# Optimization experiments

Measured on AMD Instinct MI355X. Metric: run time of the kernel, lower is better.

Reference implementation:

```python
import jax, jax.numpy as jnp
import numpy as np

C, H, W, D, M = 64, 512, 512, 4, 16


def setup_inputs() -> dict:
    key = jax.random.key(0)
    ks = jax.random.split(key, 9)
    scale = (1.0 / (C * C)) ** 0.5
    return {
        "q": jax.random.normal(ks[0], (1, 1, H, W), jnp.float32),
        "proj_w": jax.random.normal(ks[1], (C, 1, 1, 1), jnp.float32),
        "proj_b": jax.random.normal(ks[2], (C, 1, 1), jnp.float32) * 0.01,
        "spec_wr": jax.random.normal(ks[3], (D, C, C, M, M), jnp.float32) * scale,
        "spec_wi": jax.random.normal(ks[4], (D, C, C, M, M), jnp.float32) * scale,
        "w_w": jax.random.normal(ks[5], (D, C, C, 1, 1), jnp.float32) * (1.0 / C ** 0.5),
        "w_b": jax.random.normal(ks[6], (D, C, 1, 1), jnp.float32) * 0.01,
        "final_w": jax.random.normal(ks[7], (1, C, 1, 1), jnp.float32) * (1.0 / C ** 0.5),
        "final_b": jax.random.normal(ks[8], (1, 1, 1), jnp.float32) * 0.01,
    }


def _spectral(x, wr, wi, m):
    # x: (C,H,W). FFT2 -> contract low modes -> zero-pad -> iFFT2, take real part.
    Cin, Hh, Ww = x.shape
    x_ft = jnp.fft.fft2(x, axes=(-2, -1))  # (C,H,W) complex
    w = (wr + 1j * wi).astype(x_ft.dtype)  # (Cin,Cout,m,m)
    out_sub = jnp.einsum('imn,iomn->omn', x_ft[:, :m, :m], w)
    out_ft = jnp.zeros((wr.shape[1], Hh, Ww), dtype=x_ft.dtype).at[:, :m, :m].set(out_sub)
    return jnp.fft.ifft2(out_ft, axes=(-2, -1)).real


def reference(q, proj_w, proj_b, spec_wr, spec_wi, w_w, w_b, final_w, final_b):
    m = spec_wr.shape[-1]
    depth = spec_wr.shape[0]
    x = q[0].astype(jnp.float32)  # (C_in,H,W) -- batch must be 1
    # 1x1 conv lift
    x = jnp.einsum('oi,ihw->ohw', proj_w[:, :, 0, 0], x) + proj_b
    for d in range(depth):
        x_spec = _spectral(x, spec_wr[d], spec_wi[d], m)
        x_local = jnp.einsum('oi,ihw->ohw', w_w[d, :, :, 0, 0], x) + w_b[d]
        x = jax.nn.gelu(x_spec + x_local)
    x = jnp.einsum('oi,ihw->ohw', final_w[:, :, 0, 0], x) + final_b
    return x[None]  # re-add batch dim
```

## Files before the change

### kernel.cpp

```cpp
#include <hip/hip_runtime.h>
#include <cmath>

#define CC 64
#define HH 512
#define WWID 512
#define HWSZ (HH*WWID)
#define DEPTH 4

typedef __attribute__((ext_vector_type(8))) short short8;
typedef __attribute__((ext_vector_type(4))) float floatx4;

__device__ inline unsigned short f2bf(float f){
  unsigned int u = __float_as_uint(f);
  u += 0x7FFF + ((u >> 16) & 1);
  return (unsigned short)(u >> 16);
}
__device__ inline float bf2f(unsigned short h){
  return __uint_as_float(((unsigned int)h) << 16);
}

__global__ void k_init(const float* __restrict__ ww,
                       float* __restrict__ ctab, float* __restrict__ stab,
                       unsigned short* __restrict__ trigBh, unsigned short* __restrict__ trigBl,
                       unsigned short* __restrict__ trigTh, unsigned short* __restrict__ trigTl,
                       unsigned short* __restrict__ Whi, unsigned short* __restrict__ Wlo,
                       float4* __restrict__ Xfz){
  if (blockIdx.x < 32) Xfz[blockIdx.x*256 + threadIdx.x] = make_float4(0.f,0.f,0.f,0.f);
  int idx = blockIdx.x*256 + threadIdx.x;
  if (idx < 8192){
    int pos = idx >> 4, k = idx & 15;
    int r = (pos * k) & 511;
    double ang = (2.0 * 3.14159265358979323846 / 512.0) * (double)r;
    float c = (float)cos(ang), s = (float)sin(ang);
    ctab[idx] = c;  stab[idx] = s;
    unsigned short ch = f2bf(c), sh = f2bf(s);
    unsigned short cl = f2bf(c - bf2f(ch)), sl = f2bf(s - bf2f(sh));
    trigBh[pos*32 + 2*k]     = ch;  trigBl[pos*32 + 2*k]     = cl;
    trigBh[pos*32 + 2*k + 1] = sh;  trigBl[pos*32 + 2*k + 1] = sl;
    trigTh[(2*k)*512 + pos]   = ch;  trigTl[(2*k)*512 + pos]   = cl;
    trigTh[(2*k+1)*512 + pos] = sh;  trigTl[(2*k+1)*512 + pos] = sl;
  } else {
    int t = idx - 8192;
    float v = ww[t];
    unsigned short h = f2bf(v);
    Whi[t] = h;  Wlo[t] = f2bf(v - bf2f(h));
  }
}

#define APITCH 136
#define XPITCH 33
template<int LIFT>
__global__ __launch_bounds__(256) void k_dftw(const unsigned int* __restrict__ xp,
    const float* __restrict__ qsrc, const float* __restrict__ pw, const float* __restrict__ pb,
    const unsigned short* __restrict__ trigTh, const unsigned short* __restrict__ trigTl,
    const float* __restrict__ ctab, const float* __restrict__ stab,
    float* __restrict__ Xfa, float4* __restrict__ Yz){
  if (blockIdx.x < 32) Yz[blockIdx.x*256 + threadIdx.x] = make_float4(0.f,0.f,0.f,0.f);

  __shared__ unsigned short Ahs[64*APITCH], Als[64*APITCH];
  __shared__ unsigned short Bhs[32*APITCH], Bls[32*APITCH];
  __shared__ float X1s[64*XPITCH];
  int row0 = blockIdx.x * 64;
  int i  = row0 >> 9;
  int h0 = row0 & 511;
  int t = threadIdx.x;
  int g = t >> 6, lm = t & 15, lq = (t >> 4) & 3;
  float pa = 0.f, pbv = 0.f;
  if (LIFT){ pa = pw[i]; pbv = pb[i]; }

  floatx4 acc[2] = {{0.f,0.f,0.f,0.f},{0.f,0.f,0.f,0.f}};

  for (int kc = 0; kc < 4; ++kc){
    {
      int r = t >> 2, qq = t & 3;
      unsigned int* dh = (unsigned int*)&Ahs[r*APITCH + qq*32];
      unsigned int* dl = (unsigned int*)&Als[r*APITCH + qq*32];
      if (LIFT){
        const float4* src4 = (const float4*)(qsrc + (size_t)(h0 + r)*512 + kc*128 + qq*32);
        #pragma unroll
        for (int u = 0; u < 8; ++u){
          float4 v = src4[u];
          v.x = fmaf(pa, v.x, pbv); v.y = fmaf(pa, v.y, pbv);
          v.z = fmaf(pa, v.z, pbv); v.w = fmaf(pa, v.w, pbv);
          unsigned short h0_ = f2bf(v.x), h1 = f2bf(v.y), h2 = f2bf(v.z), h3 = f2bf(v.w);
          unsigned short g0 = f2bf(v.x - bf2f(h0_)), g1 = f2bf(v.y - bf2f(h1));
          unsigned short g2 = f2bf(v.z - bf2f(h2)), g3 = f2bf(v.w - bf2f(h3));
          uint2 ph, pl;
          ph.x = (unsigned)h0_ | ((unsigned)h1 << 16);
          ph.y = (unsigned)h2 | ((unsigned)h3 << 16);
          pl.x = (unsigned)g0 | ((unsigned)g1 << 16);
          pl.y = (unsigned)g2 | ((unsigned)g3 << 16);
          *(uint2*)&dh[u*2] = ph;
          *(uint2*)&dl[u*2] = pl;
        }
      } else {
        const uint4* srcp = (const uint4*)(xp + ((size_t)(h0 + r)*64 + i)*512 + kc*128 + qq*32);
        #pragma unroll
        for (int u = 0; u < 8; ++u){
          uint4 v = srcp[u];
          uint2 ph, pl;
          ph.x = (v.x & 0xffffu) | (v.y << 16);
          ph.y = (v.z & 0xffffu) | (v.w << 16);
          pl.x = (v.x >> 16) | (v.y & 0xffff0000u);
          pl.y = (v.z >> 16) | (v.w & 0xffff0000u);
          *(uint2*)&dh[u*2] = ph;
          *(uint2*)&dl[u*2] = pl;
        }
      }
    }
    {
      int j = t >> 3, qq = t & 7;
      const uint4* sh = (const uint4*)((const unsigned int*)trigTh + j*256 + kc*64 + qq*8);
      const uint4* sl = (const uint4*)((const unsigned int*)trigTl + j*256 + kc*64 + qq*8);
      uint4* dh = (uint4*)&Bhs[j*APITCH + qq*16];
      uint4* dl = (uint4*)&Bls[j*APITCH + qq*16];
      dh[0] = sh[0]; dh[1] = sh[1];
      dl[0] = sl[0]; dl[1] = sl[1];
    }
    __syncthreads();
    #pragma unroll
    for (int ks = 0; ks < 4; ++ks){
      short8 ah = *(const short8*)&Ahs[(g*16 + lm)*APITCH + ks*32 + lq*8];
      short8 al = *(const short8*)&Als[(g*16 + lm)*APITCH + ks*32 + lq*8];
      #pragma unroll
      for (int nt = 0; nt < 2; ++nt){
        short8 bh = *(const short8*)&Bhs[(nt*16 + lm)*APITCH + ks*32 + lq*8];
        short8 bl = *(const short8*)&Bls[(nt*16 + lm)*APITCH + ks*32 + lq*8];
        acc[nt] = __builtin_amdgcn_mfma_f32_16x16x32_bf16(ah, bh, acc[nt], 0, 0, 0);
        acc[nt] = __builtin_amdgcn_mfma_f32_16x16x32_bf16(ah, bl, acc[nt], 0, 0, 0);
        acc[nt] = __builtin_amdgcn_mfma_f32_16x16x32_bf16(al, bh, acc[nt], 0, 0, 0);
      }
    }
    __syncthreads();
  }
  #pragma unroll
  for (int nt = 0; nt < 2; ++nt){
    int j = nt*16 + lm;
    float sgn = (j & 1) ? -1.f : 1.f;
    #pragma unroll
    for (int rg = 0; rg < 4; ++rg){
      int m = g*16 + lq*4 + rg;
      X1s[m*XPITCH + j] = sgn * acc[nt][rg];
    }
  }
  __syncthreads();

  int mo = t >> 4, n = t & 15;
  float ar = 0.f, ai = 0.f;
  #pragma unroll 8
  for (int hh = 0; hh < 64; ++hh){
    int h = h0 + hh;
    float Re = X1s[hh*XPITCH + 2*n];
    float Im = X1s[hh*XPITCH + 2*n + 1];
    float c = ctab[h*16 + mo], s = stab[h*16 + mo];
    ar += Re*c + Im*s;
    ai += Im*c - Re*s;
  }
  atomicAdd(&Xfa[(i*256 + t)*2],     ar);
  atomicAdd(&Xfa[(i*256 + t)*2 + 1], ai);
}

__global__ void k_contract(const float2* __restrict__ Xf,
                           const float* __restrict__ wr, const float* __restrict__ wi,
                           float* __restrict__ Ya){
  int o = blockIdx.x, ic = blockIdx.y;
  int mn = blockIdx.z*64 + threadIdx.x;
  float ar = 0.f, ai = 0.f;
  int i0 = ic * 16;
  #pragma unroll
  for (int ii = 0; ii < 16; ++ii){
    int i = i0 + ii;
    float2 xf = Xf[i*256 + mn];
    float wrv = wr[(i*64 + o)*256 + mn];
    float wiv = wi[(i*64 + o)*256 + mn];
    ar += xf.x*wrv - xf.y*wiv;
    ai += xf.x*wiv + xf.y*wrv;
  }
  const float sc = 1.f/262144.f;
  atomicAdd(&Ya[(o*256 + mn)*2],     ar*sc);
  atomicAdd(&Ya[(o*256 + mn)*2 + 1], ai*sc);
}

__global__ void k_idfth(const float2* __restrict__ Y, const float* __restrict__ ct,
                        const float* __restrict__ st,
                        unsigned int* __restrict__ Thi, unsigned int* __restrict__ Tlo,
                        float4* __restrict__ Xfz){
  if (blockIdx.x < 32) Xfz[blockIdx.x*256 + threadIdx.x] = make_float4(0.f,0.f,0.f,0.f);
  int idx = blockIdx.x*256 + threadIdx.x;
  int n = idx & 15, o = (idx >> 4) & 63, h = idx >> 10;
  float ar = 0.f, ai = 0.f;
  #pragma unroll
  for (int m = 0; m < 16; ++m){
    float2 y = Y[(o<<8) + (m<<4) + n];
    float c = ct[h*16 + m], s = st[h*16 + m];
    ar += y.x*c - y.y*s;
    ai += y.x*s + y.y*c;
  }
  float tr = ar, ts = -ai;
  unsigned short rh = f2bf(tr), sh = f2bf(ts);
  Thi[idx] = (unsigned int)rh | ((unsigned int)sh << 16);
  unsigned short rl = f2bf(tr - bf2f(rh)), slr = f2bf(ts - bf2f(sh));
  Tlo[idx] = (unsigned int)rl | ((unsigned int)slr << 16);
}

#define PITCH 104
template<int LIFT, int FINAL>
__global__ __launch_bounds__(256, 4) void k_combine(
    const unsigned int* __restrict__ xp, const float* __restrict__ qsrc,
    const float* __restrict__ pw, const float* __restrict__ pb,
    const unsigned short* __restrict__ Whid, const unsigned short* __restrict__ Wlod,
    const unsigned int* __restrict__ Thi,  const unsigned int* __restrict__ Tlo,
    const unsigned short* __restrict__ trigBh, const unsigned short* __restrict__ trigBl,
    const float* __restrict__ wb, unsigned int* __restrict__ xo,
    const float* __restrict__ fw, const float* __restrict__ fb,
    float* __restrict__ outp)
{
  __shared__ unsigned short Ah[64*PITCH], Al[64*PITCH];
  int h  = blockIdx.y;
  int w0 = blockIdx.x * 128;
  int t  = threadIdx.x;

  {
    int o = t >> 2, q8 = t & 3;
    const uint4* sh = (const uint4*)((const unsigned int*)Whid + o*32 + q8*8);
    const uint4* sl = (const uint4*)((const unsigned int*)Wlod + o*32 + q8*8);
    uint4* dh = (uint4*)((unsigned int*)&Ah[o*PITCH] + q8*8);
    uint4* dl = (uint4*)((unsigned int*)&Al[o*PITCH] + q8*8);
    dh[0] = sh[0]; dh[1] = sh[1];
    dl[0] = sl[0]; dl[1] = sl[1];
  }
  {
    int o = t >> 2, q4 = t & 3;
    const uint4* sh = (const uint4*)(Thi + (size_t)h*1024 + o*16 + q4*4);
    const uint4* sl = (const uint4*)(Tlo + (size_t)h*1024 + o*16 + q4*4);
    uint4* dh = (uint4*)((unsigned int*)&Ah[o*PITCH + 64] + q4*4);
    uint4* dl = (uint4*)((unsigned int*)&Al[o*PITCH + 64] + q4*4);
    dh[0] = sh[0];
    dl[0] = sl[0];
  }
  __syncthreads();

  int g  = t >> 6;
  int lm = t & 15;
  int lq = (t >> 4) & 3;

  short8 af0 = *(const short8*)&Ah[(g*16 + lm)*PITCH +  0 + lq*8];
  short8 al0 = *(const short8*)&Al[(g*16 + lm)*PITCH +  0 + lq*8];
  short8 af1 = *(const short8*)&Ah[(g*16 + lm)*PITCH + 32 + lq*8];
  short8 al1 = *(const short8*)&Al[(g*16 + lm)*PITCH + 32 + lq*8];
  short8 af2 = *(const short8*)&Ah[(g*16 + lm)*PITCH + 64 + lq*8];
  short8 al2 = *(const short8*)&Al[(g*16 + lm)*PITCH + 64 + lq*8];

  floatx4 acc[8] = {{0.f,0.f,0.f,0.f},{0.f,0.f,0.f,0.f},{0.f,0.f,0.f,0.f},{0.f,0.f,0.f,0.f},
                    {0.f,0.f,0.f,0.f},{0.f,0.f,0.f,0.f},{0.f,0.f,0.f,0.f},{0.f,0.f,0.f,0.f}};

  const unsigned int* xw = xp + (size_t)h*32768;
  float pwv[16], pbv[16];
  if (LIFT){
    #pragma unroll
    for (int u = 0; u < 8; ++u){
      pwv[u]   = pw[lq*8 + u];      pbv[u]   = pb[lq*8 + u];
      pwv[8+u] = pw[32 + lq*8 + u]; pbv[8+u] = pb[32 + lq*8 + u];
    }
  }

  #pragma unroll
  for (int nt = 0; nt < 8; ++nt){
    int w = w0 + nt*16 + lm;
    unsigned int v0[8], v1[8];
    if (LIFT){
      float qv = qsrc[(size_t)h*512 + w];
      #pragma unroll
      for (int u = 0; u < 8; ++u){
        float a = fmaf(pwv[u], qv, pbv[u]);
        unsigned short hh = f2bf(a), ll = f2bf(a - bf2f(hh));
        v0[u] = (unsigned int)hh | ((unsigned int)ll << 16);
        float b = fmaf(pwv[8+u], qv, pbv[8+u]);
        unsigned short hb = f2bf(b), lb = f2bf(b - bf2f(hb));
        v1[u] = (unsigned int)hb | ((unsigned int)lb << 16);
      }
    } else {
      #pragma unroll
      for (int u = 0; u < 8; ++u){
        v0[u] = xw[(size_t)(     lq*8 + u)*512 + w];
        v1[u] = xw[(size_t)(32 + lq*8 + u)*512 + w];
      }
    }
    unsigned int f0[4], l0[4], f1[4], l1[4];
    #pragma unroll
    for (int p = 0; p < 4; ++p){
      f0[p] = (v0[2*p] & 0xffffu) | (v0[2*p+1] << 16);
      l0[p] = (v0[2*p] >> 16)     | (v0[2*p+1] & 0xffff0000u);
      f1[p] = (v1[2*p] & 0xffffu) | (v1[2*p+1] << 16);
      l1[p] = (v1[2*p] >> 16)     | (v1[2*p+1] & 0xffff0000u);
    }
    short8 bf0 = *(short8*)f0, bl0 = *(short8*)l0;
    short8 bf1 = *(short8*)f1, bl1 = *(short8*)l1;
    short8 bf2 = *(const short8*)(trigBh + (size_t)w*32 + lq*8);
    short8 bl2 = *(const short8*)(trigBl + (size_t)w*32 + lq*8);

    acc[nt] = __builtin_amdgcn_mfma_f32_16x16x32_bf16(af0, bf0, acc[nt], 0, 0, 0);
    acc[nt] = __builtin_amdgcn_mfma_f32_16x16x32_bf16(af0, bl0, acc[nt], 0, 0, 0);
    acc[nt] = __builtin_amdgcn_mfma_f32_16x16x32_bf16(al0, bf0, acc[nt], 0, 0, 0);
    acc[nt] = __builtin_amdgcn_mfma_f32_16x16x32_bf16(af1, bf1, acc[nt], 0, 0, 0);
    acc[nt] = __builtin_amdgcn_mfma_f32_16x16x32_bf16(af1, bl1, acc[nt], 0, 0, 0);
    acc[nt] = __builtin_amdgcn_mfma_f32_16x16x32_bf16(al1, bf1, acc[nt], 0, 0, 0);
    acc[nt] = __builtin_amdgcn_mfma_f32_16x16x32_bf16(af2, bf2, acc[nt], 0, 0, 0);
    acc[nt] = __builtin_amdgcn_mfma_f32_16x16x32_bf16(af2, bl2, acc[nt], 0, 0, 0);
    acc[nt] = __builtin_amdgcn_mfma_f32_16x16x32_bf16(al2, bf2, acc[nt], 0, 0, 0);
  }

  if (!FINAL){
    #pragma unroll
    for (int nt = 0; nt < 8; ++nt){
      int w = w0 + nt*16 + lm;
      #pragma unroll
      for (int rg = 0; rg < 4; ++rg){
        int o = g*16 + lq*4 + rg;
        float u = acc[nt][rg] + wb[o];
        float z = 0.7978845608028654f * fmaf(0.044715f, u*u*u, u);
        float e = __expf(2.f*z);
        float gl = u - __fdividef(u, e + 1.f);
        unsigned short hi_ = f2bf(gl);
        unsigned short lo_ = f2bf(gl - bf2f(hi_));
        xo[((size_t)h*64 + o)*512 + w] = (unsigned int)hi_ | ((unsigned int)lo_ << 16);
      }
    }
  } else {
    float* fred = (float*)Ah;
    __syncthreads();
    #pragma unroll
    for (int nt = 0; nt < 8; ++nt){
      float partial = 0.f;
      #pragma unroll
      for (int rg = 0; rg < 4; ++rg){
        int o = g*16 + lq*4 + rg;
        float u = acc[nt][rg] + wb[o];
        float z = 0.7978845608028654f * fmaf(0.044715f, u*u*u, u);
        float e = __expf(2.f*z);
        float gl = u - __fdividef(u, e + 1.f);
        partial = fmaf(fw[o], gl, partial);
      }
      fred[(nt*16 + lm)*17 + (t >> 4)] = partial;
    }
    __syncthreads();
    if (t < 128){
      float s = fb[0];
      #pragma unroll
      for (int k2 = 0; k2 < 16; ++k2) s += fred[t*17 + k2];
      outp[(size_t)h*512 + w0 + t] = s;
    }
  }
}

extern "C" void kernel_launch(void* const* d_in, const int* in_sizes, int n_in,
                              void* d_out, int out_size, void* d_ws, size_t ws_size,
                              hipStream_t stream) {
  const float* q       = (const float*)d_in[0];
  const float* proj_w  = (const float*)d_in[1];
  const float* proj_b  = (const float*)d_in[2];
  const float* spec_wr = (const float*)d_in[3];
  const float* spec_wi = (const float*)d_in[4];
  const float* w_w     = (const float*)d_in[5];
  const float* w_b     = (const float*)d_in[6];
  const float* final_w = (const float*)d_in[7];
  const float* final_b = (const float*)d_in[8];
  float* out = (float*)d_out;

  char* ws = (char*)d_ws;
  float*  ctab = (float*) (ws + 0);
  float*  stab = (float*) (ws + 32768);
  unsigned short* trigBh = (unsigned short*)(ws + 65536);
  unsigned short* trigBl = (unsigned short*)(ws + 98304);
  unsigned int* Thi = (unsigned int*)(ws + 131072);
  unsigned int* Tlo = (unsigned int*)(ws + 2228224);
  float*  Xf   = (float*) (ws + 4325376);
  float*  Y    = (float*) (ws + 4456448);
  unsigned int* x = (unsigned int*)(ws + 4587520);
  unsigned short* Whi = (unsigned short*)(ws + 71696384);
  unsigned short* Wlo = (unsigned short*)(ws + 71729152);
  unsigned short* trigTh = (unsigned short*)(ws + 71761920);
  unsigned short* trigTl = (unsigned short*)(ws + 71794688);

  k_init<<<96, 256, 0, stream>>>(w_w, ctab, stab, trigBh, trigBl, trigTh, trigTl,
                                 Whi, Wlo, (float4*)Xf);

  for (int d = 0; d < DEPTH; ++d){
    if (d == 0)
      k_dftw<1><<<512, 256, 0, stream>>>(x, q, proj_w, proj_b, trigTh, trigTl,
                                         ctab, stab, Xf, (float4*)Y);
    else
      k_dftw<0><<<512, 256, 0, stream>>>(x, q, proj_w, proj_b, trigTh, trigTl,
                                         ctab, stab, Xf, (float4*)Y);
    k_contract<<<dim3(64,4,4), 64, 0, stream>>>((const float2*)Xf,
                                                spec_wr + (size_t)d*1048576,
                                                spec_wi + (size_t)d*1048576, Y);
    k_idfth<<<2048, 256, 0, stream>>>((const float2*)Y, ctab, stab, Thi, Tlo,
                                      (float4*)Xf);
    if (d == 0)
      k_combine<1,0><<<dim3(4,512), 256, 0, stream>>>(x, q, proj_w, proj_b,
          Whi + d*4096, Wlo + d*4096, Thi, Tlo, trigBh, trigBl,
          w_b + d*64, x, final_w, final_b, out);
    else if (d < DEPTH-1)
      k_combine<0,0><<<dim3(4,512), 256, 0, stream>>>(x, q, proj_w, proj_b,
          Whi + d*4096, Wlo + d*4096, Thi, Tlo, trigBh, trigBl,
          w_b + d*64, x, final_w, final_b, out);
    else
      k_combine<0,1><<<dim3(4,512), 256, 0, stream>>>(x, q, proj_w, proj_b,
          Whi + d*4096, Wlo + d*4096, Thi, Tlo, trigBh, trigBl,
          w_b + d*64, x, final_w, final_b, out);
  }
}
```

Baseline: 338.7 us.

## Split waves across columns instead of output rows to avoid redundant B-fragment builds

Each wave now owns 32 columns and all 64 output channels, instead of 16 output channels across all 128 columns. This means the B fragments (x loads, bf16 splitting and trig tables) are built once per column rather than four times, one per wave. In exchange, every wave reads all A fragments from shared memory, and the occupancy hint in launch_bounds is removed, which may raise register use. The final-layer reduction is changed to sum 4 partials per column instead of 16.

After: 327.9 us. 3.2% less time.

```diff
diff --git a/kernel.cpp b/kernel.cpp
--- a/kernel.cpp
+++ b/kernel.cpp
@@ -205,7 +205,7 @@
 
 #define PITCH 104
 template<int LIFT, int FINAL>
-__global__ __launch_bounds__(256, 4) void k_combine(
+__global__ __launch_bounds__(256) void k_combine(
     const unsigned int* __restrict__ xp, const float* __restrict__ qsrc,
     const float* __restrict__ pw, const float* __restrict__ pb,
     const unsigned short* __restrict__ Whid, const unsigned short* __restrict__ Wlod,
@@ -243,16 +243,7 @@
   int g  = t >> 6;
   int lm = t & 15;
   int lq = (t >> 4) & 3;
-
-  short8 af0 = *(const short8*)&Ah[(g*16 + lm)*PITCH +  0 + lq*8];
-  short8 al0 = *(const short8*)&Al[(g*16 + lm)*PITCH +  0 + lq*8];
-  short8 af1 = *(const short8*)&Ah[(g*16 + lm)*PITCH + 32 + lq*8];
-  short8 al1 = *(const short8*)&Al[(g*16 + lm)*PITCH + 32 + lq*8];
-  short8 af2 = *(const short8*)&Ah[(g*16 + lm)*PITCH + 64 + lq*8];
-  short8 al2 = *(const short8*)&Al[(g*16 + lm)*PITCH + 64 + lq*8];
-
-  floatx4 acc[8] = {{0.f,0.f,0.f,0.f},{0.f,0.f,0.f,0.f},{0.f,0.f,0.f,0.f},{0.f,0.f,0.f,0.f},
-                    {0.f,0.f,0.f,0.f},{0.f,0.f,0.f,0.f},{0.f,0.f,0.f,0.f},{0.f,0.f,0.f,0.f}};
+  int wbase = w0 + g*32;
 
   const unsigned int* xw = xp + (size_t)h*32768;
   float pwv[16], pbv[16];
@@ -264,9 +255,10 @@
     }
   }
 
+  short8 bf0[2], bl0[2], bf1[2], bl1[2], bf2[2], bl2[2];
   #pragma unroll
-  for (int nt = 0; nt < 8; ++nt){
-    int w = w0 + nt*16 + lm;
+  for (int nt = 0; nt < 2; ++nt){
+    int w = wbase + nt*16 + lm;
     unsigned int v0[8], v1[8];
     if (LIFT){
       float qv = qsrc[(size_t)h*512 + w];
@@ -294,60 +286,83 @@
       f1[p] = (v1[2*p] & 0xffffu) | (v1[2*p+1] << 16);
       l1[p] = (v1[2*p] >> 16)     | (v1[2*p+1] & 0xffff0000u);
     }
-    short8 bf0 = *(short8*)f0, bl0 = *(short8*)l0;
-    short8 bf1 = *(short8*)f1, bl1 = *(short8*)l1;
-    short8 bf2 = *(const short8*)(trigBh + (size_t)w*32 + lq*8);
-    short8 bl2 = *(const short8*)(trigBl + (size_t)w*32 + lq*8);
-
-    acc[nt] = __builtin_amdgcn_mfma_f32_16x16x32_bf16(af0, bf0, acc[nt], 0, 0, 0);
-    acc[nt] = __builtin_amdgcn_mfma_f32_16x16x32_bf16(af0, bl0, acc[nt], 0, 0, 0);
-    acc[nt] = __builtin_amdgcn_mfma_f32_16x16x32_bf16(al0, bf0, acc[nt], 0, 0, 0);
-    acc[nt] = __builtin_amdgcn_mfma_f32_16x16x32_bf16(af1, bf1, acc[nt], 0, 0, 0);
-    acc[nt] = __builtin_amdgcn_mfma_f32_16x16x32_bf16(af1, bl1, acc[nt], 0, 0, 0);
-    acc[nt] = __builtin_amdgcn_mfma_f32_16x16x32_bf16(al1, bf1, acc[nt], 0, 0, 0);
-    acc[nt] = __builtin_amdgcn_mfma_f32_16x16x32_bf16(af2, bf2, acc[nt], 0, 0, 0);
-    acc[nt] = __builtin_amdgcn_mfma_f32_16x16x32_bf16(af2, bl2, acc[nt], 0, 0, 0);
-    acc[nt] = __builtin_amdgcn_mfma_f32_16x16x32_bf16(al2, bf2, acc[nt], 0, 0, 0);
+    bf0[nt] = *(short8*)f0;  bl0[nt] = *(short8*)l0;
+    bf1[nt] = *(short8*)f1;  bl1[nt] = *(short8*)l1;
+    bf2[nt] = *(const short8*)(trigBh + (size_t)w*32 + lq*8);
+    bl2[nt] = *(const short8*)(trigBl + (size_t)w*32 + lq*8);
+  }
+
+  floatx4 acc[8] = {{0.f,0.f,0.f,0.f},{0.f,0.f,0.f,0.f},{0.f,0.f,0.f,0.f},{0.f,0.f,0.f,0.f},
+                    {0.f,0.f,0.f,0.f},{0.f,0.f,0.f,0.f},{0.f,0.f,0.f,0.f},{0.f,0.f,0.f,0.f}};
+
+  #pragma unroll
+  for (int m = 0; m < 4; ++m){
+    short8 af0 = *(const short8*)&Ah[(m*16 + lm)*PITCH +  0 + lq*8];
+    short8 al0 = *(const short8*)&Al[(m*16 + lm)*PITCH +  0 + lq*8];
+    short8 af1 = *(const short8*)&Ah[(m*16 + lm)*PITCH + 32 + lq*8];
+    short8 al1 = *(const short8*)&Al[(m*16 + lm)*PITCH + 32 + lq*8];
+    short8 af2 = *(const short8*)&Ah[(m*16 + lm)*PITCH + 64 + lq*8];
+    short8 al2 = *(const short8*)&Al[(m*16 + lm)*PITCH + 64 + lq*8];
+    #pragma unroll
+    for (int nt = 0; nt < 2; ++nt){
+      int a = m*2 + nt;
+      acc[a] = __builtin_amdgcn_mfma_f32_16x16x32_bf16(af0, bf0[nt], acc[a], 0, 0, 0);
+      acc[a] = __builtin_amdgcn_mfma_f32_16x16x32_bf16(af0, bl0[nt], acc[a], 0, 0, 0);
+      acc[a] = __builtin_amdgcn_mfma_f32_16x16x32_bf16(al0, bf0[nt], acc[a], 0, 0, 0);
+      acc[a] = __builtin_amdgcn_mfma_f32_16x16x32_bf16(af1, bf1[nt], acc[a], 0, 0, 0);
+      acc[a] = __builtin_amdgcn_mfma_f32_16x16x32_bf16(af1, bl1[nt], acc[a], 0, 0, 0);
+      acc[a] = __builtin_amdgcn_mfma_f32_16x16x32_bf16(al1, bf1[nt], acc[a], 0, 0, 0);
+      acc[a] = __builtin_amdgcn_mfma_f32_16x16x32_bf16(af2, bf2[nt], acc[a], 0, 0, 0);
+      acc[a] = __builtin_amdgcn_mfma_f32_16x16x32_bf16(af2, bl2[nt], acc[a], 0, 0, 0);
+      acc[a] = __builtin_amdgcn_mfma_f32_16x16x32_bf16(al2, bf2[nt], acc[a], 0, 0, 0);
+    }
   }
 
   if (!FINAL){
     #pragma unroll
-    for (int nt = 0; nt < 8; ++nt){
-      int w = w0 + nt*16 + lm;
-      #pragma unroll
-      for (int rg = 0; rg < 4; ++rg){
-        int o = g*16 + lq*4 + rg;
-        float u = acc[nt][rg] + wb[o];
-        float z = 0.7978845608028654f * fmaf(0.044715f, u*u*u, u);
-        float e = __expf(2.f*z);
-        float gl = u - __fdividef(u, e + 1.f);
-        unsigned short hi_ = f2bf(gl);
-        unsigned short lo_ = f2bf(gl - bf2f(hi_));
-        xo[((size_t)h*64 + o)*512 + w] = (unsigned int)hi_ | ((unsigned int)lo_ << 16);
+    for (int m = 0; m < 4; ++m){
+      #pragma unroll
+      for (int nt = 0; nt < 2; ++nt){
+        int w = wbase + nt*16 + lm;
+        #pragma unroll
+        for (int rg = 0; rg < 4; ++rg){
+          int o = m*16 + lq*4 + rg;
+          float u = acc[m*2+nt][rg] + wb[o];
+          float z = 0.7978845608028654f * fmaf(0.044715f, u*u*u, u);
+          float e = __expf(2.f*z);
+          float gl = u - __fdividef(u, e + 1.f);
+          unsigned short hi_ = f2bf(gl);
+          unsigned short lo_ = f2bf(gl - bf2f(hi_));
+          xo[((size_t)h*64 + o)*512 + w] = (unsigned int)hi_ | ((unsigned int)lo_ << 16);
+        }
       }
     }
   } else {
     float* fred = (float*)Ah;
     __syncthreads();
     #pragma unroll
-    for (int nt = 0; nt < 8; ++nt){
+    for (int nt = 0; nt < 2; ++nt){
       float partial = 0.f;
       #pragma unroll
-      for (int rg = 0; rg < 4; ++rg){
-        int o = g*16 + lq*4 + rg;
-        float u = acc[nt][rg] + wb[o];
-        float z = 0.7978845608028654f * fmaf(0.044715f, u*u*u, u);
-        float e = __expf(2.f*z);
-        float gl = u - __fdividef(u, e + 1.f);
-        partial = fmaf(fw[o], gl, partial);
-      }
-      fred[(nt*16 + lm)*17 + (t >> 4)] = partial;
+      for (int m = 0; m < 4; ++m){
+        #pragma unroll
+        for (int rg = 0; rg < 4; ++rg){
+          int o = m*16 + lq*4 + rg;
+          float u = acc[m*2+nt][rg] + wb[o];
+          float z = 0.7978845608028654f * fmaf(0.044715f, u*u*u, u);
+          float e = __expf(2.f*z);
+          float gl = u - __fdividef(u, e + 1.f);
+          partial = fmaf(fw[o], gl, partial);
+        }
+      }
+      int wl = g*32 + nt*16 + lm;
+      fred[wl*17 + lq] = partial;
     }
     __syncthreads();
     if (t < 128){
       float s = fb[0];
       #pragma unroll
-      for (int k2 = 0; k2 < 16; ++k2) s += fred[t*17 + k2];
+      for (int k2 = 0; k2 < 4; ++k2) s += fred[t*17 + k2];
       outp[(size_t)h*512 + w0 + t] = s;
     }
   }
```
